# Performance work log

Hardware: AMD Instinct MI355X
Metric: run time of the kernel (lower is better)

The kernel has to match this reference:

```python
import jax, jax.numpy as jnp
import numpy as np

B = 4096
F_REG, F_CMP, L, D = 25, 25, 20, 64
V_REG = 50000          # regular-table vocab (table has V_REG+1 rows, row 0 = padding)
N_BUCKETS = 100000     # emb_skip_threshold -> compressed table has N_BUCKETS+1 rows


def setup_inputs() -> dict:
    key = jax.random.key(0)
    k1, k2, k3 = jax.random.split(key, 3)
    int_feats = jax.random.randint(k1, (B, (F_REG + F_CMP) * L), 0, 600000, dtype=jnp.int32)
    # xavier-normal-ish init, padding row 0 zeroed (nn.Embedding padding_idx=0)
    W_reg = jax.random.normal(k2, (F_REG, V_REG + 1, D), jnp.float32) * 0.02
    W_reg = W_reg.at[:, 0, :].set(0.0)
    W_cmp = jax.random.normal(k3, (F_CMP, N_BUCKETS + 1, D), jnp.float32) * 0.02
    W_cmp = W_cmp.at[:, 0, :].set(0.0)
    return {"int_feats": int_feats, "W_reg": W_reg, "W_cmp": W_cmp}


def _bag_mean(W, idx):
    # W: [F, V, D], idx: [B, F, L] -> mean-pooled bags [B, F, D]
    emb = jax.vmap(lambda w, i: w[i], in_axes=(0, 1), out_axes=1)(W, idx)  # [B,F,L,D]
    cnt = jnp.maximum((idx > 0).sum(-1), 1).astype(W.dtype)                # [B,F]
    return emb.sum(axis=2) / cnt[..., None]


def reference(int_feats, W_reg, W_cmp):
    b = int_feats.shape[0]
    feats = int_feats.reshape(b, F_REG + F_CMP, L)
    # regular tables: clamp(0, vocab_size)
    reg_idx = jnp.clip(feats[:, :F_REG], 0, V_REG)
    # compressed tables: clamp_min(0), then hash_compress_ids into [1, N_BUCKETS], 0 stays 0
    v = jnp.maximum(feats[:, F_REG:], 0)
    cmp_idx = jnp.where(v > 0, (jnp.maximum(v, 1) - 1) % N_BUCKETS + 1, 0)
    tokens_reg = _bag_mean(W_reg, reg_idx)   # [B, 25, D]
    tokens_cmp = _bag_mean(W_cmp, cmp_idx)   # [B, 25, D]
    return jnp.concatenate([tokens_reg, tokens_cmp], axis=1)  # [B, 50, D]
```

## Files before the change

kernel.cpp:

```cpp
#include <hip/hip_runtime.h>

constexpr int B_SZ     = 4096;
constexpr int F_REG    = 25;
constexpr int F_CMP    = 25;
constexpr int F_TOT    = F_REG + F_CMP;
constexpr int L_LEN    = 20;
constexpr int D_DIM    = 64;
constexpr int V_REG    = 50000;
constexpr int N_BUCKET = 100000;

constexpr int WAVES_PER_BLOCK = 4;

__global__ __launch_bounds__(256)
void embed_bag_kernel(const int* __restrict__ feats,
                      const float* __restrict__ Wreg,
                      const float* __restrict__ Wcmp,
                      float* __restrict__ out)
{
    const int lane = threadIdx.x & 63;
    const int wave = threadIdx.x >> 6;
    const int bag  = blockIdx.x * WAVES_PER_BLOCK + wave;
    if (bag >= B_SZ * F_TOT) return;

    const int b = bag / F_TOT;
    const int f = bag - b * F_TOT;

    const int* bag_feats = feats + (size_t)b * (F_TOT * L_LEN) + f * L_LEN;
    int idx = 0;
    if (lane < L_LEN) {
        int v = bag_feats[lane];
        if (f < F_REG) {
            idx = min(max(v, 0), V_REG);
        } else {
            v = max(v, 0);
            idx = (v > 0) ? ((v - 1) % N_BUCKET + 1) : 0;
        }
    }

    unsigned long long nz = __ballot(lane < L_LEN && idx > 0);
    int cnt = __popcll(nz);
    float cntf = (float)(cnt > 0 ? cnt : 1);

    const float* table = (f < F_REG)
        ? (Wreg + (size_t)f * (size_t)(V_REG + 1) * D_DIM)
        : (Wcmp + (size_t)(f - F_REG) * (size_t)(N_BUCKET + 1) * D_DIM);

    float acc = 0.0f;
    #pragma unroll
    for (int l = 0; l < L_LEN; ++l) {
        int rl = __shfl(idx, l, 64);
        acc += table[(size_t)rl * D_DIM + lane];
    }

    out[(size_t)bag * D_DIM + lane] = acc / cntf;
}

extern "C" void kernel_launch(void* const* d_in, const int* in_sizes, int n_in,
                              void* d_out, int out_size, void* d_ws, size_t ws_size,
                              hipStream_t stream) {
    const int*   feats = (const int*)d_in[0];
    const float* Wreg  = (const float*)d_in[1];
    const float* Wcmp  = (const float*)d_in[2];
    float*       out   = (float*)d_out;

    const int n_bags = B_SZ * F_TOT;
    const int grid   = n_bags / WAVES_PER_BLOCK;
    embed_bag_kernel<<<grid, 256, 0, stream>>>(feats, Wreg, Wcmp, out);
}
```

Before: 916.8 us.

## Stage bag indices in LDS and gather rows with float4 loads, four bags per wave

Each wave now handles four bags, with 16 lanes per bag each loading a float4 of the 64-dim row, replacing one bag per wave with scalar loads. Indices for the block's 16 bags are loaded cooperatively, clamped or hashed, and stored in shared memory, which removes the per-row shuffles and the ballot. The goal is wider, fewer memory instructions per gathered row and less latency from index handling. The cost is a block-wide sync and more registers for the unrolled row indices.

New measurement: 914.3 us. No clear change (-0.3%).

```diff
diff --git a/kernel.cpp b/kernel.cpp
--- a/kernel.cpp
+++ b/kernel.cpp
@@ -1,6 +1,5 @@
 #include <hip/hip_runtime.h>
 
-constexpr int B_SZ     = 4096;
 constexpr int F_REG    = 25;
 constexpr int F_CMP    = 25;
 constexpr int F_TOT    = F_REG + F_CMP;
@@ -9,7 +8,7 @@
 constexpr int V_REG    = 50000;
 constexpr int N_BUCKET = 100000;
 
-constexpr int WAVES_PER_BLOCK = 4;
+constexpr int BAGS_PER_BLOCK = 16;
 
 __global__ __launch_bounds__(256)
 void embed_bag_kernel(const int* __restrict__ feats,
@@ -17,42 +16,58 @@
                       const float* __restrict__ Wcmp,
                       float* __restrict__ out)
 {
-    const int lane = threadIdx.x & 63;
-    const int wave = threadIdx.x >> 6;
-    const int bag  = blockIdx.x * WAVES_PER_BLOCK + wave;
-    if (bag >= B_SZ * F_TOT) return;
+    __shared__ int s_idx[BAGS_PER_BLOCK * L_LEN];
 
-    const int b = bag / F_TOT;
-    const int f = bag - b * F_TOT;
+    const int tid        = threadIdx.x;
+    const int block_bag0 = blockIdx.x * BAGS_PER_BLOCK;
 
-    const int* bag_feats = feats + (size_t)b * (F_TOT * L_LEN) + f * L_LEN;
-    int idx = 0;
-    if (lane < L_LEN) {
-        int v = bag_feats[lane];
+    for (int s = tid; s < BAGS_PER_BLOCK * L_LEN; s += 256) {
+        int v = feats[(size_t)block_bag0 * L_LEN + s];
+        const int f = (block_bag0 + s / L_LEN) % F_TOT;
+        int idx;
         if (f < F_REG) {
             idx = min(max(v, 0), V_REG);
         } else {
             v = max(v, 0);
             idx = (v > 0) ? ((v - 1) % N_BUCKET + 1) : 0;
         }
+        s_idx[s] = idx;
+    }
+    __syncthreads();
+
+    const int lane      = tid & 63;
+    const int wave      = tid >> 6;
+    const int q         = lane >> 4;
+    const int lane16    = lane & 15;
+    const int bag_local = wave * 4 + q;
+    const int bag       = block_bag0 + bag_local;
+
+    const int f = bag % F_TOT;
+    const float* tbl = (f < F_REG)
+        ? Wreg + (size_t)f           * (size_t)(V_REG    + 1) * D_DIM
+        : Wcmp + (size_t)(f - F_REG) * (size_t)(N_BUCKET + 1) * D_DIM;
+
+    int rows[L_LEN];
+    #pragma unroll
+    for (int l = 0; l < L_LEN; ++l)
+        rows[l] = s_idx[bag_local * L_LEN + l];
+
+    int cnt = 0;
+    #pragma unroll
+    for (int l = 0; l < L_LEN; ++l)
+        cnt += (rows[l] > 0);
+
+    float4 acc = {0.0f, 0.0f, 0.0f, 0.0f};
+    #pragma unroll
+    for (int l = 0; l < L_LEN; ++l) {
+        const float4 v = *reinterpret_cast<const float4*>(
+            tbl + (size_t)rows[l] * D_DIM + lane16 * 4);
+        acc.x += v.x; acc.y += v.y; acc.z += v.z; acc.w += v.w;
     }
 
-    unsigned long long nz = __ballot(lane < L_LEN && idx > 0);
-    int cnt = __popcll(nz);
-    float cntf = (float)(cnt > 0 ? cnt : 1);
-
-    const float* table = (f < F_REG)
-        ? (Wreg + (size_t)f * (size_t)(V_REG + 1) * D_DIM)
-        : (Wcmp + (size_t)(f - F_REG) * (size_t)(N_BUCKET + 1) * D_DIM);
-
-    float acc = 0.0f;
-    #pragma unroll
-    for (int l = 0; l < L_LEN; ++l) {
-        int rl = __shfl(idx, l, 64);
-        acc += table[(size_t)rl * D_DIM + lane];
-    }
-
-    out[(size_t)bag * D_DIM + lane] = acc / cntf;
+    const float inv = 1.0f / (float)(cnt > 0 ? cnt : 1);
+    float4 r = {acc.x * inv, acc.y * inv, acc.z * inv, acc.w * inv};
+    *reinterpret_cast<float4*>(out + (size_t)bag * D_DIM + lane16 * 4) = r;
 }
 
 extern "C" void kernel_launch(void* const* d_in, const int* in_sizes, int n_in,
@@ -63,7 +78,7 @@
     const float* Wcmp  = (const float*)d_in[2];
     float*       out   = (float*)d_out;
 
-    const int n_bags = B_SZ * F_TOT;
-    const int grid   = n_bags / WAVES_PER_BLOCK;
+    const int n_bags = out_size / D_DIM;
+    const int grid   = n_bags / BAGS_PER_BLOCK;
     embed_bag_kernel<<<grid, 256, 0, stream>>>(feats, Wreg, Wcmp, out);
 }
```
